# Performance work log

Measured on AMD Instinct MI355X. Metric: run time of the kernel, lower is better.

The kernel has to match this reference:

```python
import jax, jax.numpy as jnp
import numpy as np

N_NODES = 100000
N_EDGES = 3200000
IN_FEATS = 512
HIDDEN = 256
N_CLASSES = 64
NITER = 10
HALT_BIAS_INIT = 3.0


def setup_inputs() -> dict:
    key = jax.random.key(0)
    ks = jax.random.split(key, 8)
    x = jax.random.normal(ks[0], (N_NODES, IN_FEATS), dtype=jnp.float32)
    edge_index = jax.random.randint(ks[1], (2, N_EDGES), 0, N_NODES, dtype=jnp.int64)
    # Linear layers: layers[0]: in->hidden, layers[1]: hidden->classes, halt: classes->1
    W0 = jax.random.normal(ks[2], (IN_FEATS, HIDDEN), dtype=jnp.float32) / np.sqrt(IN_FEATS)
    b0 = jnp.zeros((HIDDEN,), dtype=jnp.float32)
    W1 = jax.random.normal(ks[3], (HIDDEN, N_CLASSES), dtype=jnp.float32) / np.sqrt(HIDDEN)
    b1 = jnp.zeros((N_CLASSES,), dtype=jnp.float32)
    Wh = jax.random.normal(ks[4], (N_CLASSES, 1), dtype=jnp.float32) / np.sqrt(N_CLASSES)
    bh = jnp.full((1,), HALT_BIAS_INIT, dtype=jnp.float32)
    return {"x": x, "edge_index": edge_index, "edge_dropout": 0,
            "W0": W0, "b0": b0, "W1": W1, "b1": b1, "Wh": Wh, "bh": bh}


def reference(x, edge_index, edge_dropout, W0, b0, W1, b1, Wh, bh):
    N = x.shape[0]
    # MLP encoder (eval mode: dropout is identity)
    h = jax.nn.relu(x @ W0 + b0)
    h = h @ W1 + b1                                   # [N, C]

    # gcn_norm with self-loops (edge_dropout=0 in eval => identical every iter)
    loops = jnp.arange(N, dtype=edge_index.dtype)
    row = jnp.concatenate([edge_index[0], loops])     # source
    col = jnp.concatenate([edge_index[1], loops])     # target (aggregation index)
    deg = jax.ops.segment_sum(jnp.ones_like(col, dtype=h.dtype), col, num_segments=N)
    dinv = jnp.where(deg > 0, deg ** -0.5, 0.0)
    norm = dinv[row] * dinv[col]                      # [E+N]

    def step(ph, _):
        msg = norm[:, None] * ph[row]                 # gather + scale, [E+N, C]
        ph2 = jax.ops.segment_sum(msg, col, num_segments=N)  # scatter_add
        logit = jnp.clip(ph2 @ Wh + bh, -10.0, 10.0)  # [N, 1]
        return ph2, (ph2, logit)

    _, (props, logits) = jax.lax.scan(step, h, None, length=NITER)
    outputs = jnp.concatenate([h[None], props], axis=0)       # [niter+1, N, C]
    halting_logits = jnp.transpose(logits[:, :, 0])           # [N, niter]

    lam = jax.nn.sigmoid(halting_logits)
    remain = jnp.cumprod(1.0 - lam, axis=1)                   # inclusive
    remain_excl = jnp.concatenate([jnp.ones((N, 1), lam.dtype), remain[:, :-1]], axis=1)
    p = lam * remain_excl
    p = p.at[:, -1].add(remain[:, -1])                        # leftover mass to last step
    return outputs, p, halting_logits
```

## Files before the change

### kernel.cpp

```cpp
#include <hip/hip_runtime.h>
#include <hip/hip_bf16.h>

#define N_NODES  100000
#define N_EDGES  3200000
#define IN_FEATS 512
#define HIDDEN   256
#define N_CLASSES 64
#define NITER    10

#define SCAN_NB  49

#define OUT_P_OFF  ((size_t)(NITER + 1) * N_NODES * N_CLASSES)
#define OUT_HL_OFF (OUT_P_OFF + (size_t)N_NODES * NITER)

#define WS_META_INTS (4 * N_NODES + 128)
#define WS_CSR_OFF   ((size_t)WS_META_INTS * 4)
#define WS_W0F_OFF   (WS_CSR_OFF + (size_t)2 * N_EDGES * 4)
#define WS_W1F_OFF   (WS_W0F_OFF + 262144)
#define WS_SH0_OFF   (WS_W1F_OFF + 32768)
#define WS_SH1_OFF   (WS_SH0_OFF + (size_t)N_NODES * 64 * 2)
#define WS_NEED_W    (WS_SH0_OFF)
#define WS_NEED_BF   (WS_SH1_OFF + (size_t)N_NODES * 64 * 2)

typedef _Float16 f16x8 __attribute__((ext_vector_type(8)));
typedef _Float16 f16x4 __attribute__((ext_vector_type(4)));
typedef float    f32x4 __attribute__((ext_vector_type(4)));

__device__ __forceinline__ float bflo(unsigned v) { return __uint_as_float(v << 16); }
__device__ __forceinline__ float bfhi(unsigned v) { return __uint_as_float(v & 0xffff0000u); }
__device__ __forceinline__ unsigned short f2bf(float f) {
    unsigned u = __float_as_uint(f);
    return (unsigned short)((u + 0x7fffu + ((u >> 16) & 1u)) >> 16);
}

__global__ void k_detect(const int* ei, int* flag) {
    if (threadIdx.x == 0 && blockIdx.x == 0) {
        int is64 = 1;
        for (int k = 0; k < 128; ++k) {
            if (ei[2 * k + 1] != 0) { is64 = 0; break; }
        }
        *flag = is64;
    }
}

__device__ __forceinline__ int edge_row(const void* ei, int is64, int e) {
    return is64 ? (int)((const long long*)ei)[e] : ((const int*)ei)[e];
}
__device__ __forceinline__ int edge_col(const void* ei, int is64, int e) {
    return is64 ? (int)((const long long*)ei)[(size_t)N_EDGES + e]
                : ((const int*)ei)[(size_t)N_EDGES + e];
}

__global__ void k_count(const void* ei, const int* flag, int* cnt) {
    int e = blockIdx.x * 256 + threadIdx.x;
    if (e >= N_EDGES) return;
    int is64 = *flag;
    atomicAdd(&cnt[edge_col(ei, is64, e)], 1);
}

__global__ __launch_bounds__(256) void k_scan1(const int* cnt, int* part) {
    __shared__ int sd[256];
    int b = blockIdx.x, t = threadIdx.x;
    int s = 0;
    for (int j = t; j < 2048; j += 256) {
        int idx = b * 2048 + j;
        if (idx < N_NODES) s += cnt[idx];
    }
    sd[t] = s;
    __syncthreads();
    for (int o = 128; o > 0; o >>= 1) {
        if (t < o) sd[t] += sd[t + o];
        __syncthreads();
    }
    if (t == 0) part[b] = sd[0];
}

__global__ __launch_bounds__(256) void k_scan2(int* part, int* offs) {
    __shared__ int sd[256];
    int t = threadIdx.x;
    sd[t] = (t < SCAN_NB) ? part[t] : 0;
    __syncthreads();
    for (int o = 1; o < 256; o <<= 1) {
        int add = (t >= o) ? sd[t - o] : 0;
        __syncthreads();
        sd[t] += add;
        __syncthreads();
    }
    if (t < SCAN_NB) part[t] = (t == 0) ? 0 : sd[t - 1];
    if (t == 0) offs[N_NODES] = N_EDGES;
}

__global__ __launch_bounds__(256) void k_scan3(const int* cnt, const int* part, int* offs) {
    __shared__ int sd[256];
    int b = blockIdx.x, t = threadIdx.x;
    int base = b * 2048 + t * 8;
    int local[8];
    int s = 0;
#pragma unroll
    for (int j = 0; j < 8; ++j) {
        int idx = base + j;
        int v = (idx < N_NODES) ? cnt[idx] : 0;
        local[j] = s;
        s += v;
    }
    sd[t] = s;
    __syncthreads();
    for (int o = 1; o < 256; o <<= 1) {
        int add = (t >= o) ? sd[t - o] : 0;
        __syncthreads();
        sd[t] += add;
        __syncthreads();
    }
    int tbase = part[b] + ((t == 0) ? 0 : sd[t - 1]);
#pragma unroll
    for (int j = 0; j < 8; ++j) {
        int idx = base + j;
        if (idx < N_NODES) offs[idx] = tbase + local[j];
    }
}

__global__ void k_dinv(const int* cnt, float* dinv) {
    int i = blockIdx.x * 256 + threadIdx.x;
    if (i >= N_NODES) return;
    dinv[i] = rsqrtf((float)(cnt[i] + 1));
}

__global__ void k_fill(const void* ei, const int* flag, const float* dinv,
                       const int* offs, int* cursor, int2* csr) {
    int e = blockIdx.x * 256 + threadIdx.x;
    if (e >= N_EDGES) return;
    int is64 = *flag;
    int r = edge_row(ei, is64, e);
    int c = edge_col(ei, is64, e);
    int pos = offs[c] + atomicAdd(&cursor[c], 1);
    csr[pos] = make_int2(r, __float_as_int(dinv[r] * dinv[c]));
}

__global__ void k_prep_w(const float* __restrict__ W0, const float* __restrict__ W1,
                         _Float16* __restrict__ W0f, _Float16* __restrict__ W1f) {
    int id = blockIdx.x * 256 + threadIdx.x;
    if (id < 16384) {
        int l = id & 63, c = (id >> 6) & 15, kkg = id >> 10;
        int n = c * 16 + (l & 15);
        int kb = kkg * 32 + ((l >> 4) * 8);
        f16x8 v;
#pragma unroll
        for (int j = 0; j < 8; ++j) v[j] = (_Float16)W0[(size_t)(kb + j) * HIDDEN + n];
        *(f16x8*)&W0f[(size_t)id * 8] = v;
    } else if (id < 16384 + 2048) {
        int id2 = id - 16384;
        int l = id2 & 63, c = (id2 >> 6) & 3, kkg = id2 >> 8;
        int n = c * 16 + (l & 15);
        int kb = kkg * 32 + ((l >> 4) * 8);
        f16x8 v;
#pragma unroll
        for (int j = 0; j < 8; ++j) v[j] = (_Float16)W1[(size_t)(kb + j) * N_CLASSES + n];
        *(f16x8*)&W1f[(size_t)id2 * 8] = v;
    }
}

#define EBM 64
#define XS_STRIDE 72
#define H1_STRIDE 264
__global__ __launch_bounds__(256) void k_encoder_mfma(
        const float* __restrict__ x, const _Float16* __restrict__ W0f,
        const float* __restrict__ b0, const _Float16* __restrict__ W1f,
        const float* __restrict__ b1, float* __restrict__ out,
        unsigned short* __restrict__ shadow, int write_shadow) {
    __shared__ char smem[EBM * H1_STRIDE * 2];
    _Float16 (*h1s)[H1_STRIDE] = (_Float16(*)[H1_STRIDE])smem;
    _Float16 (*xsb[2])[XS_STRIDE];
    xsb[0] = (_Float16(*)[XS_STRIDE])smem;
    xsb[1] = (_Float16(*)[XS_STRIDE])(smem + EBM * XS_STRIDE * 2);

    const int t = threadIdx.x;
    const int w = t >> 6, l = t & 63;
    const int g = l >> 4, r15 = l & 15;
    const int row0 = blockIdx.x * EBM;
    const int srow[4] = {(0 * 256 + t) >> 4, (1 * 256 + t) >> 4,
                         (2 * 256 + t) >> 4, (3 * 256 + t) >> 4};
    const int c4 = t & 15;

    f32x4 acc[16];
#pragma unroll
    for (int c = 0; c < 16; ++c) acc[c] = (f32x4){0.f, 0.f, 0.f, 0.f};

    float4 ld[4];
#pragma unroll
    for (int q = 0; q < 4; ++q) {
        int grow = row0 + srow[q];
        if (grow >= N_NODES) grow = N_NODES - 1;
        ld[q] = *(const float4*)&x[(size_t)grow * IN_FEATS + c4 * 4];
    }
#pragma unroll
    for (int q = 0; q < 4; ++q) {
        f16x4 hv = {(_Float16)ld[q].x, (_Float16)ld[q].y, (_Float16)ld[q].z, (_Float16)ld[q].w};
        *(f16x4*)&xsb[0][srow[q]][c4 * 4] = hv;
    }

    for (int kc = 0; kc < 8; ++kc) {
        if (kc < 7) {
#pragma unroll
            for (int q = 0; q < 4; ++q) {
                int grow = row0 + srow[q];
                if (grow >= N_NODES) grow = N_NODES - 1;
                ld[q] = *(const float4*)&x[(size_t)grow * IN_FEATS + (kc + 1) * 64 + c4 * 4];
            }
        }
        __syncthreads();
        _Float16 (*xs)[XS_STRIDE] = xsb[kc & 1];
#pragma unroll
        for (int kk = 0; kk < 2; ++kk) {
            int kkg = kc * 2 + kk;
            f16x8 af = *(const f16x8*)&xs[w * 16 + r15][kk * 32 + g * 8];
#pragma unroll
            for (int c = 0; c < 16; ++c) {
                f16x8 bf = *(const f16x8*)&W0f[(size_t)((kkg * 16 + c) * 64 + l) * 8];
                acc[c] = __builtin_amdgcn_mfma_f32_16x16x32_f16(af, bf, acc[c], 0, 0, 0);
            }
        }
        if (kc < 7) {
#pragma unroll
            for (int q = 0; q < 4; ++q) {
                f16x4 hv = {(_Float16)ld[q].x, (_Float16)ld[q].y, (_Float16)ld[q].z, (_Float16)ld[q].w};
                *(f16x4*)&xsb[(kc + 1) & 1][srow[q]][c4 * 4] = hv;
            }
        }
    }
    __syncthreads();
#pragma unroll
    for (int c = 0; c < 16; ++c) {
        float bb = b0[c * 16 + r15];
#pragma unroll
        for (int i = 0; i < 4; ++i) {
            int row = w * 16 + g * 4 + i;
            h1s[row][c * 16 + r15] = (_Float16)fmaxf(acc[c][i] + bb, 0.f);
        }
    }
    __syncthreads();
    f32x4 acc2[4];
#pragma unroll
    for (int c = 0; c < 4; ++c) acc2[c] = (f32x4){0.f, 0.f, 0.f, 0.f};
#pragma unroll
    for (int kkg = 0; kkg < 8; ++kkg) {
        f16x8 af = *(const f16x8*)&h1s[w * 16 + r15][kkg * 32 + g * 8];
#pragma unroll
        for (int c = 0; c < 4; ++c) {
            f16x8 bf = *(const f16x8*)&W1f[(size_t)((kkg * 4 + c) * 64 + l) * 8];
            acc2[c] = __builtin_amdgcn_mfma_f32_16x16x32_f16(af, bf, acc2[c], 0, 0, 0);
        }
    }
#pragma unroll
    for (int c = 0; c < 4; ++c) {
        float bb = b1[c * 16 + r15];
#pragma unroll
        for (int i = 0; i < 4; ++i) {
            int row = row0 + w * 16 + g * 4 + i;
            if (row < N_NODES) {
                float v = acc2[c][i] + bb;
                int col = c * 16 + r15;
                out[(size_t)row * 64 + col] = v;
                if (write_shadow) shadow[(size_t)row * 64 + col] = f2bf(v);
            }
        }
    }
}

__global__ __launch_bounds__(256) void k_encoder(const float* __restrict__ x,
        const float* __restrict__ W0, const float* __restrict__ b0,
        const float* __restrict__ W1, const float* __restrict__ b1,
        float* __restrict__ out) {
    __shared__ float xsh[32][128];
    __shared__ float h1s[32][HIDDEN + 1];
    const int t = threadIdx.x;
    const int rg = t >> 6;
    const int cg = t & 63;
    const size_t row0 = (size_t)blockIdx.x * 32;
    float acc[8][4];
#pragma unroll
    for (int i = 0; i < 8; ++i)
        acc[i][0] = acc[i][1] = acc[i][2] = acc[i][3] = 0.f;
    for (int kc = 0; kc < 4; ++kc) {
        __syncthreads();
#pragma unroll
        for (int q = 0; q < 4; ++q) {
            int idx = t + q * 256;
            int r = idx >> 5, pos = idx & 31;
            *(float4*)&xsh[r][pos * 4] =
                *(const float4*)&x[(row0 + r) * IN_FEATS + kc * 128 + pos * 4];
        }
        __syncthreads();
        for (int kk = 0; kk < 128; kk += 4) {
            float4 xv[8];
#pragma unroll
            for (int i = 0; i < 8; ++i) xv[i] = *(const float4*)&xsh[rg * 8 + i][kk];
#pragma unroll
            for (int j = 0; j < 4; ++j) {
                float4 wv = *(const float4*)&W0[(size_t)(kc * 128 + kk + j) * HIDDEN + cg * 4];
#pragma unroll
                for (int i = 0; i < 8; ++i) {
                    float xj = (&xv[i].x)[j];
                    acc[i][0] = fmaf(xj, wv.x, acc[i][0]);
                    acc[i][1] = fmaf(xj, wv.y, acc[i][1]);
                    acc[i][2] = fmaf(xj, wv.z, acc[i][2]);
                    acc[i][3] = fmaf(xj, wv.w, acc[i][3]);
                }
            }
        }
    }
    float4 bb = *(const float4*)&b0[cg * 4];
#pragma unroll
    for (int i = 0; i < 8; ++i) {
        int r = rg * 8 + i;
        h1s[r][cg * 4 + 0] = fmaxf(acc[i][0] + bb.x, 0.f);
        h1s[r][cg * 4 + 1] = fmaxf(acc[i][1] + bb.y, 0.f);
        h1s[r][cg * 4 + 2] = fmaxf(acc[i][2] + bb.z, 0.f);
        h1s[r][cg * 4 + 3] = fmaxf(acc[i][3] + bb.w, 0.f);
    }
    __syncthreads();
    float a2[8];
#pragma unroll
    for (int i = 0; i < 8; ++i) a2[i] = 0.f;
    for (int k = 0; k < HIDDEN; ++k) {
        float wv = W1[(size_t)k * N_CLASSES + cg];
#pragma unroll
        for (int i = 0; i < 8; ++i) a2[i] = fmaf(h1s[rg * 8 + i][k], wv, a2[i]);
    }
    float bv = b1[cg];
#pragma unroll
    for (int i = 0; i < 8; ++i)
        out[(row0 + rg * 8 + i) * N_CLASSES + cg] = a2[i] + bv;
}

__global__ __launch_bounds__(256) void k_prop_bf(
        const unsigned short* __restrict__ pin_bf, float* __restrict__ pout,
        unsigned short* __restrict__ pout_bf, const int* __restrict__ offs,
        const int2* __restrict__ csr, const float* __restrict__ dinv,
        const float* __restrict__ Wh, const float* __restrict__ bh,
        float* __restrict__ hl, int t) {
    int node = (blockIdx.x * 256 + threadIdx.x) >> 5;
    if (node >= N_NODES) return;
    int hlane = threadIdx.x & 31;
    int base = threadIdx.x & 32;
    float di = dinv[node];
    unsigned vs = *(const unsigned*)&pin_bf[(size_t)node * 64 + hlane * 2];
    float a0 = di * di * bflo(vs), a1 = di * di * bfhi(vs);
    float c0 = 0.f, c1 = 0.f;
    int e0 = offs[node], e1 = offs[node + 1];
    for (int eb = e0; eb < e1; eb += 32) {
        int n = e1 - eb; if (n > 32) n = 32;
        int idx = eb + hlane;
        int2 ew = csr[idx < e1 ? idx : e1 - 1];
        int j = 0;
        for (; j + 8 <= n; j += 8) {
            unsigned v[8]; float w[8];
#pragma unroll
            for (int q = 0; q < 8; ++q) {
                int s = __shfl(ew.x, base + j + q, 64);
                w[q] = __int_as_float(__shfl(ew.y, base + j + q, 64));
                v[q] = *(const unsigned*)&pin_bf[(size_t)s * 64 + hlane * 2];
            }
#pragma unroll
            for (int q = 0; q < 8; ++q) {
                if (q & 1) { c0 = fmaf(w[q], bflo(v[q]), c0); c1 = fmaf(w[q], bfhi(v[q]), c1); }
                else       { a0 = fmaf(w[q], bflo(v[q]), a0); a1 = fmaf(w[q], bfhi(v[q]), a1); }
            }
        }
        for (; j < n; ++j) {
            int s = __shfl(ew.x, base + j, 64);
            float w = __int_as_float(__shfl(ew.y, base + j, 64));
            unsigned v = *(const unsigned*)&pin_bf[(size_t)s * 64 + hlane * 2];
            a0 = fmaf(w, bflo(v), a0);
            a1 = fmaf(w, bfhi(v), a1);
        }
    }
    float fa = a0 + c0, fb = a1 + c1;
    *(float2*)&pout[(size_t)node * 64 + hlane * 2] = make_float2(fa, fb);
    *(unsigned*)&pout_bf[(size_t)node * 64 + hlane * 2] =
        (unsigned)f2bf(fa) | ((unsigned)f2bf(fb) << 16);
    float2 wh = *(const float2*)&Wh[hlane * 2];
    float s = fa * wh.x + fb * wh.y;
#pragma unroll
    for (int o = 16; o > 0; o >>= 1) s += __shfl_xor(s, o, 64);
    if (hlane == 0) {
        float lg = s + bh[0];
        lg = fminf(10.0f, fmaxf(-10.0f, lg));
        hl[(size_t)node * NITER + t] = lg;
    }
}

__global__ __launch_bounds__(256) void k_prop(const float* __restrict__ pin,
        float* __restrict__ pout, const int* __restrict__ offs,
        const int2* __restrict__ csr, const float* __restrict__ dinv,
        const float* __restrict__ Wh, const float* __restrict__ bh,
        float* __restrict__ hl, int t) {
    int wid = (blockIdx.x * blockDim.x + threadIdx.x) >> 6;
    int lane = threadIdx.x & 63;
    if (wid >= N_NODES) return;
    float di = dinv[wid];
    float a[4];
    a[0] = di * di * pin[(size_t)wid * 64 + lane];
    a[1] = a[2] = a[3] = 0.f;
    int e0 = offs[wid], e1 = offs[wid + 1];
    for (int eb = e0; eb < e1; eb += 64) {
        int n = e1 - eb; if (n > 64) n = 64;
        int idx = eb + lane;
        int2 ew = csr[idx < e1 ? idx : e1 - 1];
        int j = 0;
        for (; j + 8 <= n; j += 8) {
            float v[8], w[8];
#pragma unroll
            for (int q = 0; q < 8; ++q) {
                int s = __shfl(ew.x, j + q, 64);
                w[q] = __int_as_float(__shfl(ew.y, j + q, 64));
                v[q] = pin[(size_t)s * 64 + lane];
            }
#pragma unroll
            for (int q = 0; q < 8; ++q) a[q & 3] = fmaf(w[q], v[q], a[q & 3]);
        }
        for (; j < n; ++j) {
            int s = __shfl(ew.x, j, 64);
            float w = __int_as_float(__shfl(ew.y, j, 64));
            a[0] = fmaf(w, pin[(size_t)s * 64 + lane], a[0]);
        }
    }
    float acc = (a[0] + a[1]) + (a[2] + a[3]);
    pout[(size_t)wid * 64 + lane] = acc;
    float s = acc * Wh[lane];
#pragma unroll
    for (int o = 32; o > 0; o >>= 1) s += __shfl_xor(s, o, 64);
    if (lane == 0) {
        float lg = s + bh[0];
        lg = fminf(10.0f, fmaxf(-10.0f, lg));
        hl[(size_t)wid * NITER + t] = lg;
    }
}

__global__ void k_p(const float* __restrict__ hl, float* __restrict__ p) {
    int i = blockIdx.x * 256 + threadIdx.x;
    if (i >= N_NODES) return;
    float remain = 1.0f;
    float pv[NITER];
#pragma unroll
    for (int t = 0; t < NITER; ++t) {
        float lg = hl[(size_t)i * NITER + t];
        float lam = 1.0f / (1.0f + expf(-lg));
        pv[t] = lam * remain;
        remain *= (1.0f - lam);
    }
    pv[NITER - 1] += remain;
#pragma unroll
    for (int t = 0; t < NITER; ++t) p[(size_t)i * NITER + t] = pv[t];
}

extern "C" void kernel_launch(void* const* d_in, const int* in_sizes, int n_in,
                              void* d_out, int out_size, void* d_ws, size_t ws_size,
                              hipStream_t stream) {
    const float* x  = (const float*)d_in[0];
    const void*  ei = d_in[1];
    const float* W0 = (const float*)d_in[3];
    const float* b0 = (const float*)d_in[4];
    const float* W1 = (const float*)d_in[5];
    const float* b1 = (const float*)d_in[6];
    const float* Wh = (const float*)d_in[7];
    const float* bh = (const float*)d_in[8];
    float* out = (float*)d_out;

    int* ws_i   = (int*)d_ws;
    int* cnt    = ws_i;
    int* offs   = ws_i + N_NODES;
    int* cursor = ws_i + 2 * N_NODES + 2;
    int* part   = ws_i + 3 * N_NODES + 2;
    int* flag   = ws_i + 3 * N_NODES + 66;
    float* dinv = (float*)(ws_i + 3 * N_NODES + 128);
    int2* csr   = (int2*)((char*)d_ws + WS_CSR_OFF);
    _Float16* W0f = (_Float16*)((char*)d_ws + WS_W0F_OFF);
    _Float16* W1f = (_Float16*)((char*)d_ws + WS_W1F_OFF);
    unsigned short* sh0 = (unsigned short*)((char*)d_ws + WS_SH0_OFF);
    unsigned short* sh1 = (unsigned short*)((char*)d_ws + WS_SH1_OFF);

    const int use_w  = ws_size >= WS_NEED_W;
    const int use_bf = ws_size >= WS_NEED_BF;

    hipMemsetAsync(d_ws, 0, (size_t)(3 * N_NODES + 128) * 4, stream);
    k_detect<<<1, 64, 0, stream>>>((const int*)ei, flag);
    k_count<<<(N_EDGES + 255) / 256, 256, 0, stream>>>(ei, flag, cnt);
    k_scan1<<<SCAN_NB, 256, 0, stream>>>(cnt, part);
    k_scan2<<<1, 256, 0, stream>>>(part, offs);
    k_scan3<<<SCAN_NB, 256, 0, stream>>>(cnt, part, offs);
    k_dinv<<<(N_NODES + 255) / 256, 256, 0, stream>>>(cnt, dinv);
    k_fill<<<(N_EDGES + 255) / 256, 256, 0, stream>>>(ei, flag, dinv, offs, cursor, csr);

    if (use_w) {
        k_prep_w<<<72, 256, 0, stream>>>(W0, W1, W0f, W1f);
        k_encoder_mfma<<<(N_NODES + EBM - 1) / EBM, 256, 0, stream>>>(
            x, W0f, b0, W1f, b1, out, sh0, use_bf);
    } else {
        k_encoder<<<N_NODES / 32, 256, 0, stream>>>(x, W0, b0, W1, b1, out);
    }

    float* hl = out + OUT_HL_OFF;
    if (use_bf) {
        for (int it = 0; it < NITER; ++it) {
            const unsigned short* pin_bf = (it & 1) ? sh1 : sh0;
            unsigned short* pout_bf      = (it & 1) ? sh0 : sh1;
            float* pout = out + (size_t)(it + 1) * N_NODES * N_CLASSES;
            k_prop_bf<<<((size_t)N_NODES * 32 + 255) / 256, 256, 0, stream>>>(
                pin_bf, pout, pout_bf, offs, csr, dinv, Wh, bh, hl, it);
        }
    } else {
        for (int it = 0; it < NITER; ++it) {
            const float* pin = out + (size_t)it * N_NODES * N_CLASSES;
            float* pout      = out + (size_t)(it + 1) * N_NODES * N_CLASSES;
            k_prop<<<((size_t)N_NODES * 64 + 255) / 256, 256, 0, stream>>>(
                pin, pout, offs, csr, dinv, Wh, bh, hl, it);
        }
    }
    k_p<<<(N_NODES + 255) / 256, 256, 0, stream>>>(hl, out + OUT_P_OFF);
}
```

Baseline: 1.175 ms.

## Stage encoder weight fragments through double-buffered LDS instead of direct global loads

The MFMA encoder kernel previously read W0/W1 B-fragments from global memory (L2) inside the inner MFMA loop, once per wave. Now each block cooperatively loads one k-slice of weights into a double-buffered LDS region with register prefetch of the next slice, and waves read fragments from LDS. This cuts redundant global/L2 traffic across the 4 waves, at the cost of a barrier per k-step and a larger shared-memory footprint (51 KB), which may reduce occupancy. The encoder is only part of total time, which is dominated by propagation.

After: 1.020 ms. 13.2% less time.

```diff
diff --git a/kernel.cpp b/kernel.cpp
--- a/kernel.cpp
+++ b/kernel.cpp
@@ -162,93 +162,118 @@
 #define EBM 64
 #define XS_STRIDE 72
 #define H1_STRIDE 264
+#define XS0   0
+#define XS1   9216
+#define WST0  18432
+#define WST1  34816
+#define W2ST0 34816
+#define W2ST1 38912
 __global__ __launch_bounds__(256) void k_encoder_mfma(
         const float* __restrict__ x, const _Float16* __restrict__ W0f,
         const float* __restrict__ b0, const _Float16* __restrict__ W1f,
         const float* __restrict__ b1, float* __restrict__ out,
         unsigned short* __restrict__ shadow, int write_shadow) {
-    __shared__ char smem[EBM * H1_STRIDE * 2];
-    _Float16 (*h1s)[H1_STRIDE] = (_Float16(*)[H1_STRIDE])smem;
-    _Float16 (*xsb[2])[XS_STRIDE];
-    xsb[0] = (_Float16(*)[XS_STRIDE])smem;
-    xsb[1] = (_Float16(*)[XS_STRIDE])(smem + EBM * XS_STRIDE * 2);
-
+    __shared__ char smem[51200];
     const int t = threadIdx.x;
     const int w = t >> 6, l = t & 63;
     const int g = l >> 4, r15 = l & 15;
     const int row0 = blockIdx.x * EBM;
-    const int srow[4] = {(0 * 256 + t) >> 4, (1 * 256 + t) >> 4,
-                         (2 * 256 + t) >> 4, (3 * 256 + t) >> 4};
     const int c4 = t & 15;
+    const int srow0 = t >> 4;
 
     f32x4 acc[16];
 #pragma unroll
     for (int c = 0; c < 16; ++c) acc[c] = (f32x4){0.f, 0.f, 0.f, 0.f};
 
-    float4 ld[4];
+    float4 xld[4];
+    f16x8 wld[4];
 #pragma unroll
     for (int q = 0; q < 4; ++q) {
-        int grow = row0 + srow[q];
+        int grow = row0 + q * 16 + srow0;
         if (grow >= N_NODES) grow = N_NODES - 1;
-        ld[q] = *(const float4*)&x[(size_t)grow * IN_FEATS + c4 * 4];
-    }
+        xld[q] = *(const float4*)&x[(size_t)grow * IN_FEATS + c4 * 4];
+    }
+#pragma unroll
+    for (int q = 0; q < 4; ++q) wld[q] = *(const f16x8*)&W0f[(size_t)(q * 256 + t) * 8];
 #pragma unroll
     for (int q = 0; q < 4; ++q) {
-        f16x4 hv = {(_Float16)ld[q].x, (_Float16)ld[q].y, (_Float16)ld[q].z, (_Float16)ld[q].w};
-        *(f16x4*)&xsb[0][srow[q]][c4 * 4] = hv;
-    }
-
-    for (int kc = 0; kc < 8; ++kc) {
-        if (kc < 7) {
+        f16x4 hv = {(_Float16)xld[q].x, (_Float16)xld[q].y, (_Float16)xld[q].z, (_Float16)xld[q].w};
+        *(f16x4*)(smem + XS0 + ((q * 16 + srow0) * XS_STRIDE + c4 * 4) * 2) = hv;
+    }
+#pragma unroll
+    for (int q = 0; q < 4; ++q)
+        *(f16x8*)(smem + WST0 + (q * 256 + t) * 16) = wld[q];
+    __syncthreads();
+
+    for (int kkg = 0; kkg < 16; ++kkg) {
+        const int kc = kkg >> 1, kk = kkg & 1;
+        if (kkg < 15) {
+#pragma unroll
+            for (int q = 0; q < 4; ++q)
+                wld[q] = *(const f16x8*)&W0f[(size_t)((kkg + 1) * 1024 + q * 256 + t) * 8];
+        }
+        if (kk == 0 && kc < 7) {
 #pragma unroll
             for (int q = 0; q < 4; ++q) {
-                int grow = row0 + srow[q];
+                int grow = row0 + q * 16 + srow0;
                 if (grow >= N_NODES) grow = N_NODES - 1;
-                ld[q] = *(const float4*)&x[(size_t)grow * IN_FEATS + (kc + 1) * 64 + c4 * 4];
-            }
-        }
-        __syncthreads();
-        _Float16 (*xs)[XS_STRIDE] = xsb[kc & 1];
-#pragma unroll
-        for (int kk = 0; kk < 2; ++kk) {
-            int kkg = kc * 2 + kk;
-            f16x8 af = *(const f16x8*)&xs[w * 16 + r15][kk * 32 + g * 8];
-#pragma unroll
-            for (int c = 0; c < 16; ++c) {
-                f16x8 bf = *(const f16x8*)&W0f[(size_t)((kkg * 16 + c) * 64 + l) * 8];
-                acc[c] = __builtin_amdgcn_mfma_f32_16x16x32_f16(af, bf, acc[c], 0, 0, 0);
-            }
-        }
-        if (kc < 7) {
+                xld[q] = *(const float4*)&x[(size_t)grow * IN_FEATS + (kc + 1) * 64 + c4 * 4];
+            }
+        }
+        const char* xbase = smem + ((kc & 1) ? XS1 : XS0);
+        const char* wbase = smem + ((kkg & 1) ? WST1 : WST0);
+        f16x8 af = *(const f16x8*)(xbase + ((w * 16 + r15) * XS_STRIDE + kk * 32 + g * 8) * 2);
+#pragma unroll
+        for (int c = 0; c < 16; ++c) {
+            f16x8 bf = *(const f16x8*)(wbase + ((c << 6) | l) * 16);
+            acc[c] = __builtin_amdgcn_mfma_f32_16x16x32_f16(af, bf, acc[c], 0, 0, 0);
+        }
+        if (kkg < 15) {
+            char* wdst = smem + ((kkg & 1) ? WST0 : WST1);
+#pragma unroll
+            for (int q = 0; q < 4; ++q)
+                *(f16x8*)(wdst + (q * 256 + t) * 16) = wld[q];
+        }
+        if (kk == 1 && kc < 7) {
+            char* xdst = smem + ((kc & 1) ? XS0 : XS1);
 #pragma unroll
             for (int q = 0; q < 4; ++q) {
-                f16x4 hv = {(_Float16)ld[q].x, (_Float16)ld[q].y, (_Float16)ld[q].z, (_Float16)ld[q].w};
-                *(f16x4*)&xsb[(kc + 1) & 1][srow[q]][c4 * 4] = hv;
-            }
-        }
-    }
-    __syncthreads();
+                f16x4 hv = {(_Float16)xld[q].x, (_Float16)xld[q].y, (_Float16)xld[q].z, (_Float16)xld[q].w};
+                *(f16x4*)(xdst + ((q * 16 + srow0) * XS_STRIDE + c4 * 4) * 2) = hv;
+            }
+        }
+        __syncthreads();
+    }
+
+    f16x8 w2ld = *(const f16x8*)&W1f[(size_t)t * 8];
 #pragma unroll
     for (int c = 0; c < 16; ++c) {
         float bb = b0[c * 16 + r15];
 #pragma unroll
         for (int i = 0; i < 4; ++i) {
             int row = w * 16 + g * 4 + i;
-            h1s[row][c * 16 + r15] = (_Float16)fmaxf(acc[c][i] + bb, 0.f);
-        }
-    }
+            *(_Float16*)(smem + (row * H1_STRIDE + c * 16 + r15) * 2) =
+                (_Float16)fmaxf(acc[c][i] + bb, 0.f);
+        }
+    }
+    *(f16x8*)(smem + W2ST0 + t * 16) = w2ld;
     __syncthreads();
+
     f32x4 acc2[4];
 #pragma unroll
     for (int c = 0; c < 4; ++c) acc2[c] = (f32x4){0.f, 0.f, 0.f, 0.f};
-#pragma unroll
     for (int kkg = 0; kkg < 8; ++kkg) {
-        f16x8 af = *(const f16x8*)&h1s[w * 16 + r15][kkg * 32 + g * 8];
+        if (kkg < 7) w2ld = *(const f16x8*)&W1f[(size_t)((kkg + 1) * 256 + t) * 8];
+        const char* wbase = smem + ((kkg & 1) ? W2ST1 : W2ST0);
+        f16x8 af = *(const f16x8*)(smem + ((w * 16 + r15) * H1_STRIDE + kkg * 32 + g * 8) * 2);
 #pragma unroll
         for (int c = 0; c < 4; ++c) {
-            f16x8 bf = *(const f16x8*)&W1f[(size_t)((kkg * 4 + c) * 64 + l) * 8];
+            f16x8 bf = *(const f16x8*)(wbase + ((c << 6) | l) * 16);
             acc2[c] = __builtin_amdgcn_mfma_f32_16x16x32_f16(af, bf, acc2[c], 0, 0, 0);
         }
+        if (kkg < 7)
+            *(f16x8*)(smem + ((kkg & 1) ? W2ST0 : W2ST1) + t * 16) = w2ld;
+        __syncthreads();
     }
 #pragma unroll
     for (int c = 0; c < 4; ++c) {
```
